# Kernel tuning notes

Measured on AMD Instinct MI355X. Metric: run time of the kernel, lower is better.

## Reference

```python
import jax, jax.numpy as jnp
import numpy as np

N = 100000
E = 3200000
F_IN = 128
H = 64


def _glorot(key, fan_in, fan_out):
    lim = jnp.sqrt(6.0 / (fan_in + fan_out))
    return jax.random.uniform(key, (fan_in, fan_out), minval=-lim, maxval=lim, dtype=jnp.float32)


def setup_inputs() -> dict:
    key = jax.random.key(0)
    ks = jax.random.split(key, 16)
    x = jax.random.normal(ks[0], (N, F_IN), dtype=jnp.float32)
    edge_index = jax.random.randint(ks[1], (2, E), 0, N, dtype=jnp.int32)
    batch = jnp.zeros((N,), dtype=jnp.int32)
    dims = [(F_IN, H), (H, H // 2), (H // 2, H // 4), (H // 4, H // 2), (H // 2, H), (H, F_IN)]
    params = {}
    for i, (fi, fo) in enumerate(dims):
        params[f"W{i+1}"] = _glorot(ks[2 + i], fi, fo)
        params[f"b{i+1}"] = jnp.zeros((fo,), dtype=jnp.float32)
    params["Wf"] = _glorot(ks[10], F_IN, F_IN)
    params["bf"] = jnp.zeros((F_IN,), dtype=jnp.float32)
    return {"x": x, "edge_index": edge_index, "batch": batch, **params}


def _gcn_norm(edge_index, num_nodes):
    # PyG GCNConv: add self-loops, sym-normalize with deg^{-1/2}
    loop = jnp.arange(num_nodes, dtype=edge_index.dtype)
    row = jnp.concatenate([edge_index[0], loop])  # source j
    col = jnp.concatenate([edge_index[1], loop])  # target i
    deg = jax.ops.segment_sum(jnp.ones_like(col, dtype=jnp.float32), col, num_segments=num_nodes)
    dinv = jnp.where(deg > 0, jax.lax.rsqrt(deg), 0.0)
    norm = dinv[row] * dinv[col]
    return row, col, norm


def _gcn_conv(h, W, b, row, col, norm, num_nodes):
    h = h @ W  # linear first (no bias in lin), then normalized scatter-add
    msg = h[row] * norm[:, None]
    agg = jax.ops.segment_sum(msg, col, num_segments=num_nodes)
    return agg + b


def reference(x, edge_index, batch, W1, b1, W2, b2, W3, b3, W4, b4, W5, b5, W6, b6, Wf, bf):
    n = x.shape[0]
    row, col, norm = _gcn_norm(edge_index, n)
    h = jax.nn.relu(_gcn_conv(x, W1, b1, row, col, norm, n))
    h = jax.nn.relu(_gcn_conv(h, W2, b2, row, col, norm, n))
    h = jax.nn.relu(_gcn_conv(h, W3, b3, row, col, norm, n))
    h = jax.nn.relu(_gcn_conv(h, W4, b4, row, col, norm, n))
    h = jax.nn.relu(_gcn_conv(h, W5, b5, row, col, norm, n))
    h = jax.nn.relu(_gcn_conv(h, W6, b6, row, col, norm, n))
    return h @ Wf + bf
```

## Files before the change

### kernel.cpp

```cpp
#include <hip/hip_runtime.h>
#include <hip/hip_fp16.h>

#define BLK 256
#define NBSHIFT 9
#define MAXNB 200
#define GPART 512

typedef _Float16 half4v __attribute__((ext_vector_type(4)));
typedef _Float16 half8v __attribute__((ext_vector_type(8)));
typedef float    f32x4v __attribute__((ext_vector_type(4)));

__device__ __forceinline__ float4 ld4(const float* p) { return *(const float4*)p; }

__global__ __launch_bounds__(BLK) void p1_hist_k(const int* __restrict__ cols, int* __restrict__ hist,
                                                 int E, int nb) {
    __shared__ int h[MAXNB];
    const int tid = threadIdx.x, g = blockIdx.x;
    for (int b = tid; b < nb; b += BLK) h[b] = 0;
    __syncthreads();
    const int chunk = (E + GPART - 1) / GPART;
    const int start = g * chunk, end = min(E, start + chunk);
    for (int e = start + tid; e < end; e += BLK) atomicAdd(&h[cols[e] >> NBSHIFT], 1);
    __syncthreads();
    for (int b = tid; b < nb; b += BLK) hist[b * GPART + g] = h[b];
}
__global__ __launch_bounds__(256) void p2a_k(const int* __restrict__ hist, int* __restrict__ bstart,
                                             int nb, int E) {
    __shared__ int s[256];
    const int t = threadIdx.x;
    int tot = 0;
    if (t < nb) {
        const int* hp = &hist[t * GPART];
        for (int g = 0; g < GPART; g++) tot += hp[g];
    }
    s[t] = tot;
    __syncthreads();
    for (int o = 1; o < 256; o <<= 1) {
        int v = s[t] + ((t >= o) ? s[t - o] : 0);
        __syncthreads();
        s[t] = v;
        __syncthreads();
    }
    if (t < nb) bstart[t] = s[t] - tot;
    if (t == 0) bstart[nb] = E;
}
__global__ __launch_bounds__(256) void p2b_k(int* __restrict__ hist, const int* __restrict__ bstart) {
    __shared__ int s[GPART];
    const int b = blockIdx.x, t = threadIdx.x;
    const int v0 = hist[b * GPART + t], v1 = hist[b * GPART + 256 + t];
    s[t] = v0; s[256 + t] = v1;
    __syncthreads();
    for (int o = 1; o < GPART; o <<= 1) {
        const int a0 = s[t] + ((t >= o) ? s[t - o] : 0);
        const int a1 = s[256 + t] + ((256 + t >= o) ? s[256 + t - o] : 0);
        __syncthreads();
        s[t] = a0; s[256 + t] = a1;
        __syncthreads();
    }
    const int base = bstart[b];
    hist[b * GPART + t] = base + s[t] - v0;
    hist[b * GPART + 256 + t] = base + s[256 + t] - v1;
}
__global__ __launch_bounds__(BLK) void p3_part_k(const int* __restrict__ rows, const int* __restrict__ cols,
                                                 const int* __restrict__ hist, int2* __restrict__ pairs,
                                                 int E, int nb) {
    __shared__ int tail[MAXNB];
    const int tid = threadIdx.x, g = blockIdx.x;
    for (int b = tid; b < nb; b += BLK) tail[b] = hist[b * GPART + g];
    __syncthreads();
    const int chunk = (E + GPART - 1) / GPART;
    const int start = g * chunk, end = min(E, start + chunk);
    for (int e = start + tid; e < end; e += BLK) {
        const int r = rows[e], c = cols[e];
        const int pos = atomicAdd(&tail[c >> NBSHIFT], 1);
        pairs[pos] = make_int2(r, c);
    }
}
__global__ __launch_bounds__(BLK) void p4_fill_k(const int2* __restrict__ pairs, const int* __restrict__ bstart,
                                                 int* __restrict__ P, float* __restrict__ dinv,
                                                 int* __restrict__ srow, int n) {
    __shared__ int dh[1 << NBSHIFT];
    __shared__ int tl[1 << NBSHIFT];
    const int b = blockIdx.x, t = threadIdx.x;
    const int base = b << NBSHIFT;
    const int nnod = min(1 << NBSHIFT, n - base);
    const int lo = bstart[b], hi = bstart[b + 1];
    dh[t] = 0; dh[256 + t] = 0;
    __syncthreads();
    for (int e = lo + t; e < hi; e += BLK) atomicAdd(&dh[pairs[e].y - base], 1);
    __syncthreads();
    const int v0 = dh[t], v1 = dh[256 + t];
    tl[t] = v0; tl[256 + t] = v1;
    __syncthreads();
    for (int o = 1; o < (1 << NBSHIFT); o <<= 1) {
        const int a0 = tl[t] + ((t >= o) ? tl[t - o] : 0);
        const int a1 = tl[256 + t] + ((256 + t >= o) ? tl[256 + t - o] : 0);
        __syncthreads();
        tl[t] = a0; tl[256 + t] = a1;
        __syncthreads();
    }
    const int s0 = lo + tl[t] - v0;
    const int s1 = lo + tl[256 + t] - v1;
    __syncthreads();
    tl[t] = s0; tl[256 + t] = s1;
    if (t < nnod)       { P[base + t] = s0;       dinv[base + t] = rsqrtf((float)v0 + 1.0f); }
    if (256 + t < nnod) { P[base + 256 + t] = s1; dinv[base + 256 + t] = rsqrtf((float)v1 + 1.0f); }
    __syncthreads();
    for (int e = lo + t; e < hi; e += BLK) {
        const int2 pr = pairs[e];
        const int pos = atomicAdd(&tl[pr.y - base], 1);
        srow[pos] = pr.x;
    }
}

__device__ __forceinline__ void addh(float2 A[4], const __half* p) {
    const float4 raw = ld4((const float*)p);
    const __half2* h = (const __half2*)&raw;
    const float2 f0 = __half22float2(h[0]);
    const float2 f1 = __half22float2(h[1]);
    const float2 f2 = __half22float2(h[2]);
    const float2 f3 = __half22float2(h[3]);
    A[0].x += f0.x; A[0].y += f0.y;
    A[1].x += f1.x; A[1].y += f1.y;
    A[2].x += f2.x; A[2].y += f2.y;
    A[3].x += f3.x; A[3].y += f3.y;
}

template<int WD, bool PRE, bool OUTH>
__global__ __launch_bounds__(BLK) void gatherh_k(const __half* __restrict__ Tp, const int* __restrict__ P,
                                                 const int* __restrict__ srow, const float* __restrict__ dinv,
                                                 const float* __restrict__ bin, void* __restrict__ outv,
                                                 int n, int E) {
    constexpr int LPN = WD / 8;
    const long gid = (long)blockIdx.x * BLK + threadIdx.x;
    const int i = (int)(gid / LPN);
    if (i >= n) return;
    const int q = (int)(gid % LPN) * 8;
    const int start = P[i];
    const int end = (i + 1 < n) ? P[i + 1] : E;
    const float d = dinv[i];
    const __half* __restrict__ Tq = Tp + q;
    float2 A0[4], A1[4], A2[4], A3[4];
    {
        const float4 raw = ld4((const float*)(Tq + (long)i * WD));
        const __half2* h = (const __half2*)&raw;
        A0[0] = __half22float2(h[0]); A0[1] = __half22float2(h[1]);
        A0[2] = __half22float2(h[2]); A0[3] = __half22float2(h[3]);
    }
#pragma unroll
    for (int k = 0; k < 4; k++) {
        A1[k] = make_float2(0.f, 0.f); A2[k] = make_float2(0.f, 0.f); A3[k] = make_float2(0.f, 0.f);
    }
    int e = start;
    const int ea = min(end, (start + 3) & ~3);
    for (; e < ea; e++) addh(A0, Tq + (long)srow[e] * WD);
    for (; e + 8 <= end; e += 8) {
        const int4 j0 = *(const int4*)&srow[e];
        const int4 j1 = *(const int4*)&srow[e + 4];
        addh(A0, Tq + (long)j0.x * WD); addh(A1, Tq + (long)j0.y * WD);
        addh(A2, Tq + (long)j0.z * WD); addh(A3, Tq + (long)j0.w * WD);
        addh(A0, Tq + (long)j1.x * WD); addh(A1, Tq + (long)j1.y * WD);
        addh(A2, Tq + (long)j1.z * WD); addh(A3, Tq + (long)j1.w * WD);
    }
    if (e + 4 <= end) {
        const int4 j0 = *(const int4*)&srow[e];
        addh(A0, Tq + (long)j0.x * WD); addh(A1, Tq + (long)j0.y * WD);
        addh(A2, Tq + (long)j0.z * WD); addh(A3, Tq + (long)j0.w * WD);
        e += 4;
    }
    for (; e < end; e++) addh(A0, Tq + (long)srow[e] * WD);
#pragma unroll
    for (int k = 0; k < 4; k++) {
        A0[k].x += A1[k].x + A2[k].x + A3[k].x;
        A0[k].y += A1[k].y + A2[k].y + A3[k].y;
    }
    float v[8];
    v[0] = d * A0[0].x; v[1] = d * A0[0].y; v[2] = d * A0[1].x; v[3] = d * A0[1].y;
    v[4] = d * A0[2].x; v[5] = d * A0[2].y; v[6] = d * A0[3].x; v[7] = d * A0[3].y;
    if (PRE) {
        const float4 b0 = ld4(&bin[q]);
        const float4 b1 = ld4(&bin[q + 4]);
        v[0] = fmaxf(v[0] + b0.x, 0.f) * d; v[1] = fmaxf(v[1] + b0.y, 0.f) * d;
        v[2] = fmaxf(v[2] + b0.z, 0.f) * d; v[3] = fmaxf(v[3] + b0.w, 0.f) * d;
        v[4] = fmaxf(v[4] + b1.x, 0.f) * d; v[5] = fmaxf(v[5] + b1.y, 0.f) * d;
        v[6] = fmaxf(v[6] + b1.z, 0.f) * d; v[7] = fmaxf(v[7] + b1.w, 0.f) * d;
    }
    if (OUTH) {
        const __half2 h0 = __floats2half2_rn(v[0], v[1]);
        const __half2 h1 = __floats2half2_rn(v[2], v[3]);
        const __half2 h2 = __floats2half2_rn(v[4], v[5]);
        const __half2 h3 = __floats2half2_rn(v[6], v[7]);
        uint4 u;
        u.x = *(const unsigned int*)&h0; u.y = *(const unsigned int*)&h1;
        u.z = *(const unsigned int*)&h2; u.w = *(const unsigned int*)&h3;
        *(uint4*)((__half*)outv + (long)i * WD + q) = u;
    } else {
        float* out = (float*)outv;
        float4 v0, v1;
        v0.x = v[0]; v0.y = v[1]; v0.z = v[2]; v0.w = v[3];
        v1.x = v[4]; v1.y = v[5]; v1.z = v[6]; v1.w = v[7];
        *(float4*)&out[(long)i * WD + q] = v0;
        *(float4*)&out[(long)i * WD + q + 4] = v1;
    }
}

template<int FI, int FO, bool INB, bool OUTB, bool OUTRELU, bool OSC, bool OUTH>
__global__ __launch_bounds__(BLK) void gemm_k(const float* __restrict__ H, const float* __restrict__ Wm,
                                              const float* __restrict__ bin, const float* __restrict__ bout,
                                              const float* __restrict__ dinv, float* __restrict__ out, int n) {
    constexpr int COLT = FO / 4;
    constexpr int RTH  = BLK / COLT;
    constexpr int RPT  = (FO >= 64) ? 8 : 4;
    constexpr int ROWS = RTH * RPT;
    constexpr int KC   = (FI > 64) ? 64 : FI;
    constexpr int NKB  = FI / KC;

    __shared__ float Wl[KC * FO];
    __shared__ float Hl[ROWS * (KC + 1)];

    const int tid    = threadIdx.x;
    const int colIdx = tid % COLT;
    const int rowIdx = tid / COLT;
    const long rowBase = (long)blockIdx.x * ROWS;

    float4 acc[RPT];
#pragma unroll
    for (int i = 0; i < RPT; i++) acc[i] = make_float4(0.f, 0.f, 0.f, 0.f);

    for (int kb = 0; kb < NKB; kb++) {
        if (kb) __syncthreads();
        for (int f = tid * 4; f < KC * FO; f += BLK * 4) {
            const int kr = f / FO, c = f % FO;
            *(float4*)&Wl[kr * FO + c] = ld4(&Wm[(kb * KC + kr) * FO + c]);
        }
        for (int f = tid * 4; f < ROWS * KC; f += BLK * 4) {
            const int rr = f / KC, kk = f % KC;
            const long r = rowBase + rr;
            float4 v = make_float4(0.f, 0.f, 0.f, 0.f);
            if (r < n) v = ld4(&H[r * FI + kb * KC + kk]);
            if (INB) {
                float4 b4 = ld4(&bin[kb * KC + kk]);
                v.x = fmaxf(v.x + b4.x, 0.f); v.y = fmaxf(v.y + b4.y, 0.f);
                v.z = fmaxf(v.z + b4.z, 0.f); v.w = fmaxf(v.w + b4.w, 0.f);
            }
            float* dst = &Hl[rr * (KC + 1) + kk];
            dst[0] = v.x; dst[1] = v.y; dst[2] = v.z; dst[3] = v.w;
        }
        __syncthreads();
#pragma unroll 8
        for (int k = 0; k < KC; k++) {
            const float4 w4 = *(const float4*)&Wl[k * FO + 4 * colIdx];
#pragma unroll
            for (int i = 0; i < RPT; i++) {
                const float hv = Hl[(rowIdx * RPT + i) * (KC + 1) + k];
                acc[i].x = fmaf(hv, w4.x, acc[i].x);
                acc[i].y = fmaf(hv, w4.y, acc[i].y);
                acc[i].z = fmaf(hv, w4.z, acc[i].z);
                acc[i].w = fmaf(hv, w4.w, acc[i].w);
            }
        }
    }

    float4 bo = make_float4(0.f, 0.f, 0.f, 0.f);
    if (OUTB) bo = ld4(&bout[4 * colIdx]);
#pragma unroll
    for (int i = 0; i < RPT; i++) {
        const long r = rowBase + rowIdx * RPT + i;
        if (r < n) {
            float4 v = acc[i];
            if (OUTB) { v.x += bo.x; v.y += bo.y; v.z += bo.z; v.w += bo.w; }
            if (OUTRELU) {
                v.x = fmaxf(v.x, 0.f); v.y = fmaxf(v.y, 0.f);
                v.z = fmaxf(v.z, 0.f); v.w = fmaxf(v.w, 0.f);
            }
            if (OSC) {
                const float d = dinv[r];
                v.x *= d; v.y *= d; v.z *= d; v.w *= d;
            }
            if (OUTH) {
                const __half2 h01 = __floats2half2_rn(v.x, v.y);
                const __half2 h23 = __floats2half2_rn(v.z, v.w);
                uint2 u;
                u.x = *(const unsigned int*)&h01;
                u.y = *(const unsigned int*)&h23;
                *(uint2*)((__half*)out + r * FO + 4 * colIdx) = u;
            } else {
                *(float4*)&out[r * FO + 4 * colIdx] = v;
            }
        }
    }
}

template<int K, int FO>
__global__ __launch_bounds__(BLK) void wprep_k(const float* __restrict__ Wm, _Float16* __restrict__ Wh) {
    const int f = (blockIdx.x * BLK + threadIdx.x) * 4;
    if (f >= K * FO) return;
    const int nn = f / K, k0 = f % K;
    const int blk = k0 & ~31, g = (k0 >> 2) & 3, h = (k0 >> 4) & 1;
    half4v w4;
#pragma unroll
    for (int c = 0; c < 4; c++) w4[c] = (_Float16)Wm[(k0 + c) * FO + nn];
    *(half4v*)&Wh[nn * K + blk + 8 * g + 4 * h] = w4;
}

template<int K, int FO, bool AH, bool OUTB, bool OUTRELU, bool OSC, bool OUTH>
__global__ __launch_bounds__(BLK) void mgemm_k(const void* __restrict__ Hv, const _Float16* __restrict__ Wh,
                                               const float* __restrict__ bout, const float* __restrict__ dinv,
                                               void* __restrict__ outv, int n) {
    constexpr int BM = 64;
    constexpr int KP = K + 8;
    constexpr int NT = FO / 16;
    __shared__ _Float16 Al[BM * KP];
    __shared__ _Float16 Bl[FO * KP];

    const int tid = threadIdx.x;
    const long rowBase = (long)blockIdx.x * BM;

    for (int f = tid * 8; f < K * FO; f += BLK * 8) {
        const int nn = f / K, k = f % K;
        *(uint4*)&Bl[nn * KP + k] = *(const uint4*)&Wh[f];
    }
    if (AH) {
        const __half* Hp = (const __half*)Hv;
        for (int f = tid * 8; f < BM * K; f += BLK * 8) {
            const int rr = f / K, k0 = f % K;
            const long r = rowBase + rr;
            uint4 u = make_uint4(0u, 0u, 0u, 0u);
            if (r < n) u = *(const uint4*)&Hp[r * K + k0];
            const int blk = k0 & ~31, g0 = (k0 >> 2) & 3, h = (k0 >> 4) & 1;
            *(uint2*)&Al[rr * KP + blk + 8 * g0 + 4 * h] = make_uint2(u.x, u.y);
            *(uint2*)&Al[rr * KP + blk + 8 * (g0 + 1) + 4 * h] = make_uint2(u.z, u.w);
        }
    } else {
        const float* Hp = (const float*)Hv;
        for (int f = tid * 4; f < BM * K; f += BLK * 4) {
            const int rr = f / K, k0 = f % K;
            const long r = rowBase + rr;
            float4 v = make_float4(0.f, 0.f, 0.f, 0.f);
            if (r < n) v = ld4(&Hp[r * K + k0]);
            const int blk = k0 & ~31, g = (k0 >> 2) & 3, h = (k0 >> 4) & 1;
            half4v a4;
            a4[0] = (_Float16)v.x; a4[1] = (_Float16)v.y; a4[2] = (_Float16)v.z; a4[3] = (_Float16)v.w;
            *(half4v*)&Al[rr * KP + blk + 8 * g + 4 * h] = a4;
        }
    }
    __syncthreads();

    const int wv = tid >> 6;
    const int lane = tid & 63;
    const int lr = lane & 15;
    const int lg = lane >> 4;
    const int wrow = wv * 16;

    const f32x4v vzero = {0.f, 0.f, 0.f, 0.f};
    f32x4v acc[NT];
#pragma unroll
    for (int t = 0; t < NT; t++) acc[t] = vzero;

#pragma unroll
    for (int ks = 0; ks < K / 32; ks++) {
        const int ko = ks * 32 + 8 * lg;
        const half8v a = *(const half8v*)&Al[(wrow + lr) * KP + ko];
#pragma unroll
        for (int nt = 0; nt < NT; nt++) {
            const half8v b = *(const half8v*)&Bl[(nt * 16 + lr) * KP + ko];
            acc[nt] = __builtin_amdgcn_mfma_f32_16x16x32_f16(a, b, acc[nt], 0, 0, 0);
        }
    }

    float bo[NT];
    if (OUTB) {
#pragma unroll
        for (int nt = 0; nt < NT; nt++) bo[nt] = bout[nt * 16 + lr];
    }
#pragma unroll
    for (int r = 0; r < 4; r++) {
        const long row = rowBase + wrow + lg * 4 + r;
        if (row < n) {
            const float d = OSC ? dinv[row] : 1.0f;
#pragma unroll
            for (int nt = 0; nt < NT; nt++) {
                float v = acc[nt][r];
                if (OUTB) v += bo[nt];
                if (OUTRELU) v = fmaxf(v, 0.f);
                if (OSC) v *= d;
                if (OUTH) ((__half*)outv)[row * FO + nt * 16 + lr] = __float2half_rn(v);
                else      ((float*)outv)[row * FO + nt * 16 + lr] = v;
            }
        }
    }
}

extern "C" void kernel_launch(void* const* d_in, const int* in_sizes, int n_in,
                              void* d_out, int out_size, void* d_ws, size_t ws_size,
                              hipStream_t stream)
{
    const float* x  = (const float*)d_in[0];
    const int*   ei = (const int*)d_in[1];
    const float* W1 = (const float*)d_in[3];  const float* b1 = (const float*)d_in[4];
    const float* W2 = (const float*)d_in[5];  const float* b2 = (const float*)d_in[6];
    const float* W3 = (const float*)d_in[7];  const float* b3 = (const float*)d_in[8];
    const float* W4 = (const float*)d_in[9];  const float* b4 = (const float*)d_in[10];
    const float* W5 = (const float*)d_in[11]; const float* b5 = (const float*)d_in[12];
    const float* W6 = (const float*)d_in[13]; const float* b6 = (const float*)d_in[14];
    const float* Wf = (const float*)d_in[15]; const float* bf = (const float*)d_in[16];

    const int n = in_sizes[0] / 128;
    const int E = in_sizes[1] / 2;
    const int* rows = ei;
    const int* cols = ei + E;

    int*   P    = (int*)d_ws;
    int*   srow = P + n;
    float* dinv = (float*)(srow + E);
    float* bufA = dinv + n;
    float* bufB = bufA + (size_t)n * 128;
    int2*  pairs = (int2*)bufA;
    int*   hist  = (int*)bufB;
    int*   bstart= hist + MAXNB * GPART;
    _Float16* Wh1 = (_Float16*)(bufB + (size_t)n * 64);
    _Float16* Wh6 = Wh1 + 128 * 64;
    _Float16* Whf = Wh6 + 64 * 128;

    auto cdiv = [](long a, long b) { return (unsigned)((a + b - 1) / b); };
    const int nb = (n + (1 << NBSHIFT) - 1) >> NBSHIFT;

    wprep_k<128, 64><<<cdiv(128 * 64 / 4, BLK), BLK, 0, stream>>>(W1, Wh1);
    wprep_k<64, 128><<<cdiv(64 * 128 / 4, BLK), BLK, 0, stream>>>(W6, Wh6);
    wprep_k<128, 128><<<cdiv(128 * 128 / 4, BLK), BLK, 0, stream>>>(Wf, Whf);

    p1_hist_k<<<GPART, BLK, 0, stream>>>(cols, hist, E, nb);
    p2a_k<<<1, 256, 0, stream>>>(hist, bstart, nb, E);
    p2b_k<<<nb, 256, 0, stream>>>(hist, bstart);
    p3_part_k<<<GPART, BLK, 0, stream>>>(rows, cols, hist, pairs, E, nb);
    p4_fill_k<<<nb, BLK, 0, stream>>>(pairs, bstart, P, dinv, srow, n);

    mgemm_k<128, 64, false, false, false, true, true><<<cdiv(n, 64), BLK, 0, stream>>>(x, Wh1, nullptr, dinv, bufA, n);
    gatherh_k<64, false, false><<<cdiv((long)n * 8, BLK), BLK, 0, stream>>>((const __half*)bufA, P, srow, dinv, nullptr, bufB, n, E);

    gemm_k<64, 32, true, false, false, true, true><<<cdiv(n, 128), BLK, 0, stream>>>(bufB, W2, b1, nullptr, dinv, bufA, n);
    gatherh_k<32, false, false><<<cdiv((long)n * 4, BLK), BLK, 0, stream>>>((const __half*)bufA, P, srow, dinv, nullptr, bufB, n, E);

    gemm_k<32, 16, true, false, false, true, true><<<cdiv(n, 256), BLK, 0, stream>>>(bufB, W3, b2, nullptr, dinv, bufA, n);
    gatherh_k<16, true, true><<<cdiv((long)n * 2, BLK), BLK, 0, stream>>>((const __half*)bufA, P, srow, dinv, b3, bufB, n, E);

    gatherh_k<16, false, false><<<cdiv((long)n * 2, BLK), BLK, 0, stream>>>((const __half*)bufB, P, srow, dinv, nullptr, bufA, n, E);
    gemm_k<16, 32, false, true, true, true, true><<<cdiv(n, 128), BLK, 0, stream>>>(bufA, W4, nullptr, b4, dinv, bufB, n);

    gatherh_k<32, false, false><<<cdiv((long)n * 4, BLK), BLK, 0, stream>>>((const __half*)bufB, P, srow, dinv, nullptr, bufA, n, E);
    gemm_k<32, 64, false, true, true, true, true><<<cdiv(n, 128), BLK, 0, stream>>>(bufA, W5, nullptr, b5, dinv, bufB, n);

    gatherh_k<64, false, true><<<cdiv((long)n * 8, BLK), BLK, 0, stream>>>((const __half*)bufB, P, srow, dinv, nullptr, bufA, n, E);
    mgemm_k<64, 128, true, true, true, false, true><<<cdiv(n, 64), BLK, 0, stream>>>(bufA, Wh6, b6, nullptr, bufB, n);

    mgemm_k<128, 128, true, true, false, false, false><<<cdiv(n, 64), BLK, 0, stream>>>(bufB, Whf, bf, nullptr, d_out, n);
}
```

Before: 611.1 us.

## Shrink CSR build buckets to 128 nodes and parallelize bucket totals

Node buckets for the edge counting sort shrink from 512 to 128 nodes, so nb grows from about 196 to about 782 and the per-bucket fill kernel gets more blocks with smaller shared-memory scans. The single-block serial reduction of bucket totals is split into a parallel per-bucket reduction kernel plus a one-block scan that handles four buckets per thread. In exchange, the partition kernel's shared histogram and atomics spread over more bins, p2b launches more blocks, and there is one extra kernel launch.

```diff
diff --git a/kernel.cpp b/kernel.cpp
--- a/kernel.cpp
+++ b/kernel.cpp
@@ -2,8 +2,8 @@
 #include <hip/hip_fp16.h>
 
 #define BLK 256
-#define NBSHIFT 9
-#define MAXNB 200
+#define NBSHIFT 7
+#define MAXNB 800
 #define GPART 512
 
 typedef _Float16 half4v __attribute__((ext_vector_type(4)));
@@ -24,24 +24,41 @@
     __syncthreads();
     for (int b = tid; b < nb; b += BLK) hist[b * GPART + g] = h[b];
 }
-__global__ __launch_bounds__(256) void p2a_k(const int* __restrict__ hist, int* __restrict__ bstart,
-                                             int nb, int E) {
+__global__ __launch_bounds__(256) void p2a_tot_k(const int* __restrict__ hist, int* __restrict__ tot) {
+    __shared__ int s[256];
+    const int b = blockIdx.x, t = threadIdx.x;
+    s[t] = hist[b * GPART + t] + hist[b * GPART + 256 + t];
+    __syncthreads();
+    for (int o = 128; o > 0; o >>= 1) {
+        if (t < o) s[t] += s[t + o];
+        __syncthreads();
+    }
+    if (t == 0) tot[b] = s[0];
+}
+__global__ __launch_bounds__(256) void p2a_scan_k(const int* __restrict__ tot, int* __restrict__ bstart,
+                                                  int nb, int E) {
     __shared__ int s[256];
     const int t = threadIdx.x;
-    int tot = 0;
-    if (t < nb) {
-        const int* hp = &hist[t * GPART];
-        for (int g = 0; g < GPART; g++) tot += hp[g];
-    }
-    s[t] = tot;
+    const int base = t * 4;
+    int l0 = 0, l1 = 0, l2 = 0, l3 = 0;
+    if (base < nb)     l0 = tot[base];
+    if (base + 1 < nb) l1 = tot[base + 1];
+    if (base + 2 < nb) l2 = tot[base + 2];
+    if (base + 3 < nb) l3 = tot[base + 3];
+    const int sum = l0 + l1 + l2 + l3;
+    s[t] = sum;
     __syncthreads();
     for (int o = 1; o < 256; o <<= 1) {
-        int v = s[t] + ((t >= o) ? s[t - o] : 0);
+        const int v = s[t] + ((t >= o) ? s[t - o] : 0);
         __syncthreads();
         s[t] = v;
         __syncthreads();
     }
-    if (t < nb) bstart[t] = s[t] - tot;
+    const int excl = s[t] - sum;
+    if (base < nb)     bstart[base]     = excl;
+    if (base + 1 < nb) bstart[base + 1] = excl + l0;
+    if (base + 2 < nb) bstart[base + 2] = excl + l0 + l1;
+    if (base + 3 < nb) bstart[base + 3] = excl + l0 + l1 + l2;
     if (t == 0) bstart[nb] = E;
 }
 __global__ __launch_bounds__(256) void p2b_k(int* __restrict__ hist, const int* __restrict__ bstart) {
@@ -79,32 +96,31 @@
 __global__ __launch_bounds__(BLK) void p4_fill_k(const int2* __restrict__ pairs, const int* __restrict__ bstart,
                                                  int* __restrict__ P, float* __restrict__ dinv,
                                                  int* __restrict__ srow, int n) {
-    __shared__ int dh[1 << NBSHIFT];
-    __shared__ int tl[1 << NBSHIFT];
+    constexpr int NN = 1 << NBSHIFT;
+    __shared__ int dh[NN];
+    __shared__ int tl[NN];
     const int b = blockIdx.x, t = threadIdx.x;
     const int base = b << NBSHIFT;
-    const int nnod = min(1 << NBSHIFT, n - base);
+    const int nnod = min(NN, n - base);
     const int lo = bstart[b], hi = bstart[b + 1];
-    dh[t] = 0; dh[256 + t] = 0;
+    if (t < NN) dh[t] = 0;
     __syncthreads();
     for (int e = lo + t; e < hi; e += BLK) atomicAdd(&dh[pairs[e].y - base], 1);
     __syncthreads();
-    const int v0 = dh[t], v1 = dh[256 + t];
-    tl[t] = v0; tl[256 + t] = v1;
-    __syncthreads();
-    for (int o = 1; o < (1 << NBSHIFT); o <<= 1) {
-        const int a0 = tl[t] + ((t >= o) ? tl[t - o] : 0);
-        const int a1 = tl[256 + t] + ((256 + t >= o) ? tl[256 + t - o] : 0);
-        __syncthreads();
-        tl[t] = a0; tl[256 + t] = a1;
-        __syncthreads();
-    }
-    const int s0 = lo + tl[t] - v0;
-    const int s1 = lo + tl[256 + t] - v1;
-    __syncthreads();
-    tl[t] = s0; tl[256 + t] = s1;
-    if (t < nnod)       { P[base + t] = s0;       dinv[base + t] = rsqrtf((float)v0 + 1.0f); }
-    if (256 + t < nnod) { P[base + 256 + t] = s1; dinv[base + 256 + t] = rsqrtf((float)v1 + 1.0f); }
+    const int v0 = (t < NN) ? dh[t] : 0;
+    if (t < NN) tl[t] = v0;
+    __syncthreads();
+    for (int o = 1; o < NN; o <<= 1) {
+        int a0 = 0;
+        if (t < NN) a0 = tl[t] + ((t >= o) ? tl[t - o] : 0);
+        __syncthreads();
+        if (t < NN) tl[t] = a0;
+        __syncthreads();
+    }
+    const int s0 = lo + ((t < NN) ? tl[t] : 0) - v0;
+    __syncthreads();
+    if (t < NN) tl[t] = s0;
+    if (t < nnod) { P[base + t] = s0; dinv[base + t] = rsqrtf((float)v0 + 1.0f); }
     __syncthreads();
     for (int e = lo + t; e < hi; e += BLK) {
         const int2 pr = pairs[e];
@@ -418,6 +434,7 @@
     int2*  pairs = (int2*)bufA;
     int*   hist  = (int*)bufB;
     int*   bstart= hist + MAXNB * GPART;
+    int*   tot   = bstart + 1032;
     _Float16* Wh1 = (_Float16*)(bufB + (size_t)n * 64);
     _Float16* Wh6 = Wh1 + 128 * 64;
     _Float16* Whf = Wh6 + 64 * 128;
@@ -430,7 +447,8 @@
     wprep_k<128, 128><<<cdiv(128 * 128 / 4, BLK), BLK, 0, stream>>>(Wf, Whf);
 
     p1_hist_k<<<GPART, BLK, 0, stream>>>(cols, hist, E, nb);
-    p2a_k<<<1, 256, 0, stream>>>(hist, bstart, nb, E);
+    p2a_tot_k<<<nb, 256, 0, stream>>>(hist, tot);
+    p2a_scan_k<<<1, 256, 0, stream>>>(tot, bstart, nb, E);
     p2b_k<<<nb, 256, 0, stream>>>(hist, bstart);
     p3_part_k<<<GPART, BLK, 0, stream>>>(rows, cols, hist, pairs, E, nb);
     p4_fill_k<<<nb, BLK, 0, stream>>>(pairs, bstart, P, dinv, srow, n);
```

Measured after the change: 600.2 us. No clear change (-1.8%).
